# Kernel tuning notes

Measured on AMD Instinct MI355X. Metric: run time of the kernel, lower is better.

## Reference

```python
import jax, jax.numpy as jnp
import numpy as np

D_MODEL = 1024
NUM_HEADS = 16
DEPTH = D_MODEL // NUM_HEADS


def setup_inputs() -> dict:
    key = jax.random.key(0)
    ks = jax.random.split(key, 9)
    B, S = 2, 2048
    scale = 1.0 / np.sqrt(D_MODEL)
    x = jax.random.normal(ks[0], (B, S, D_MODEL), dtype=jnp.float32)
    wq = jax.random.normal(ks[1], (D_MODEL, D_MODEL), dtype=jnp.float32) * scale
    bq = jax.random.normal(ks[2], (D_MODEL,), dtype=jnp.float32) * 0.01
    wk = jax.random.normal(ks[3], (D_MODEL, D_MODEL), dtype=jnp.float32) * scale
    bk = jax.random.normal(ks[4], (D_MODEL,), dtype=jnp.float32) * 0.01
    wv = jax.random.normal(ks[5], (D_MODEL, D_MODEL), dtype=jnp.float32) * scale
    bv = jax.random.normal(ks[6], (D_MODEL,), dtype=jnp.float32) * 0.01
    wo = jax.random.normal(ks[7], (D_MODEL, D_MODEL), dtype=jnp.float32) * scale
    bo = jax.random.normal(ks[8], (D_MODEL,), dtype=jnp.float32) * 0.01
    return {"x": x, "wq": wq, "bq": bq, "wk": wk, "bk": bk,
            "wv": wv, "bv": bv, "wo": wo, "bo": bo}


def reference(x, wq, bq, wk, bk, wv, bv, wo, bo):
    B, S, _ = x.shape
    def split_heads(t):  # [B,S,D] -> [B,H,S,depth]
        return t.reshape(B, S, NUM_HEADS, DEPTH).transpose(0, 2, 1, 3)
    q = split_heads(x @ wq + bq)
    k = split_heads(x @ wk + bk)
    v = split_heads(x @ wv + bv)
    # scaled dot-product attention, full [B,H,S,S] scores as in the original
    logits = jnp.einsum('bhqd,bhkd->bhqk', q, k) / jnp.sqrt(
        jnp.asarray(DEPTH, dtype=jnp.float32))
    attn = jax.nn.softmax(logits, axis=-1)
    out = jnp.einsum('bhqk,bhkd->bhqd', attn, v)
    out = out.transpose(0, 2, 1, 3).reshape(B, S, D_MODEL)
    return out @ wo + bo
```

## Files before the change

kernel.cpp:

```cpp
#include <hip/hip_runtime.h>


#define S_LEN 2048
#define DM 1024
#define MROWS 4096
#define QSCALE 0.1803368801111244f

typedef unsigned short u16;
typedef unsigned int u32;
typedef __attribute__((ext_vector_type(8))) short short8;
typedef __attribute__((ext_vector_type(4))) float f32x4;
typedef __attribute__((ext_vector_type(4))) unsigned short u16x4;
typedef __attribute__((ext_vector_type(2))) unsigned int u32x2;

__device__ inline u16 f2bf(float f) {
    u32 u = __float_as_uint(f);
    u = u + 0x7fffu + ((u >> 16) & 1u);
    return (u16)(u >> 16);
}
__device__ inline void gld_lds16(const u16* g, u16* l) {
    __builtin_amdgcn_global_load_lds(
        (const __attribute__((address_space(1))) void*)g,
        (__attribute__((address_space(3))) void*)l, 16, 0, 0);
}
__device__ inline f32x4 mfma16(short8 a, short8 b, f32x4 c) {
    return __builtin_amdgcn_mfma_f32_16x16x32_bf16(a, b, c, 0, 0, 0);
}

__global__ void prep_all(const float* __restrict__ x, u16* __restrict__ xb,
                         const float* __restrict__ wq, const float* __restrict__ wk,
                         const float* __restrict__ wv, const float* __restrict__ wo,
                         const float* __restrict__ bq, const float* __restrict__ bk,
                         const float* __restrict__ bv, const float* __restrict__ bo,
                         u16* __restrict__ wallT, u16* __restrict__ woT,
                         float* __restrict__ biasAll, float* __restrict__ biasO) {
    const int t = threadIdx.x;
    if (blockIdx.x < 2048) {
        const size_t i8 = ((size_t)blockIdx.x * 256 + t) * 8;
        const f32x4 a = ((const f32x4*)x)[i8 / 4];
        const f32x4 b = ((const f32x4*)x)[i8 / 4 + 1];
        u16 o[8];
#pragma unroll
        for (int i = 0; i < 4; i++) { o[i] = f2bf(a[i]); o[4 + i] = f2bf(b[i]); }
        *(short8*)(xb + i8) = *(const short8*)o;
        return;
    }
    const int bid = blockIdx.x - 2048;
    if (bid == 1024) {
#pragma unroll
        for (int i = 0; i < 4; i++) {
            const int idx = i * 256 + t;
            biasAll[idx]        = bq[idx] * QSCALE;
            biasAll[1024 + idx] = bk[idx];
            biasAll[2048 + idx] = bv[idx];
            biasO[idx]          = bo[idx];
        }
        return;
    }
    __shared__ float lds[64][65];
    const int m  = bid >> 8;
    const int tk = (bid >> 4) & 15;
    const int tn = bid & 15;
    const float* src = (m == 0) ? wq : (m == 1) ? wk : (m == 2) ? wv : wo;
    const float scale = (m == 0) ? QSCALE : 1.0f;
    const int r4 = t >> 6, c = t & 63;
#pragma unroll
    for (int i = 0; i < 16; i++) {
        const int k = tk * 64 + i * 4 + r4;
        lds[i * 4 + r4][c] = src[(size_t)k * 1024 + tn * 64 + c];
    }
    __syncthreads();
#pragma unroll
    for (int i = 0; i < 16; i++) {
        const int n = tn * 64 + i * 4 + r4;
        const int k = tk * 64 + c;
        const u16 v = f2bf(lds[c][i * 4 + r4] * scale);
        if (m < 3) wallT[((size_t)m * 1024 + n) * 1024 + k] = v;
        else       woT[(size_t)n * 1024 + k] = v;
    }
}

__global__ __launch_bounds__(256, 3)
void gemm_qkv(const u16* __restrict__ A, const u16* __restrict__ Bt,
              const float* __restrict__ bias, u16* __restrict__ Cq,
              u16* __restrict__ Ck, u16* __restrict__ Cv,
              const int K, const int N) {
    __shared__ __align__(16) u16 As[128 * 32];
    __shared__ __align__(16) u16 Bs[128 * 32];
    __shared__ __align__(16) u16 Ct[128 * 136];
    const int tid = threadIdx.x;
    const int w = tid >> 6, lane = tid & 63;
    const int wm = w >> 1, wn = w & 1;
    const int l16 = lane & 15, quad = lane >> 4;
    const int tm = blockIdx.x * 128;
    const int tn = blockIdx.y * 128;
    const int region = tn >> 10;

    const int sr = w * 16 + (lane >> 2);
    const int sc = (lane & 3) * 8;
    const u16* ag0 = A + (size_t)(tm + sr) * K + sc;
    const u16* ag1 = A + (size_t)(tm + sr + 64) * K + sc;
    const u16* bg0 = Bt + (size_t)(tn + sr) * K + sc;
    const u16* bg1 = Bt + (size_t)(tn + sr + 64) * K + sc;
    u16* al = As + w * 512;
    u16* bl = Bs + w * 512;

    f32x4 acc[4][4];
#pragma unroll
    for (int i = 0; i < 4; i++)
#pragma unroll
        for (int j = 0; j < 4; j++) acc[i][j] = (f32x4){0.f, 0.f, 0.f, 0.f};

    for (int kb = 0; kb < K; kb += 32) {
        __syncthreads();
        gld_lds16(ag0 + kb, al);
        gld_lds16(ag1 + kb, al + 2048);
        gld_lds16(bg0 + kb, bl);
        gld_lds16(bg1 + kb, bl + 2048);
        __syncthreads();
        short8 af[4], bfr[4];
#pragma unroll
        for (int i = 0; i < 4; i++) {
            af[i]  = *(const short8*)(As + (wm * 64 + i * 16 + l16) * 32 + quad * 8);
            bfr[i] = *(const short8*)(Bs + (wn * 64 + i * 16 + l16) * 32 + quad * 8);
        }
#pragma unroll
        for (int i = 0; i < 4; i++)
#pragma unroll
            for (int j = 0; j < 4; j++)
                acc[i][j] = mfma16(af[i], bfr[j], acc[i][j]);
    }

    if (region < 2) {
#pragma unroll
        for (int j = 0; j < 4; j++) {
            const int colL = wn * 64 + j * 16 + l16;
            const float bv = bias[tn + colL];
#pragma unroll
            for (int i = 0; i < 4; i++) {
                const int row0 = wm * 64 + i * 16 + quad * 4;
#pragma unroll
                for (int r = 0; r < 4; r++)
                    Ct[(row0 + r) * 136 + colL] = f2bf(acc[i][j][r] + bv);
            }
        }
    } else {
#pragma unroll
        for (int j = 0; j < 4; j++) {
            const int colL = wn * 64 + j * 16 + l16;
            const float bv = bias[tn + colL];
#pragma unroll
            for (int i = 0; i < 4; i++) {
                const int row0 = wm * 64 + i * 16 + quad * 4;
                u16x4 pk;
#pragma unroll
                for (int r = 0; r < 4; r++) pk[r] = f2bf(acc[i][j][r] + bv);
                *(u16x4*)(Ct + colL * 132 + row0) = pk;
            }
        }
    }
    __syncthreads();

    if (region == 0) {
#pragma unroll
        for (int p = 0; p < 8; p++) {
            const int rowL = p * 16 + (tid >> 4);
            const int c8 = (tid & 15) * 8;
            const short8 v = *(const short8*)(Ct + rowL * 136 + c8);
            *(short8*)(Cq + (size_t)(tm + rowL) * 1024 + tn + c8) = v;
        }
    } else if (region == 1) {
        const int b = tm >> 11, sBase = tm & 2047;
#pragma unroll
        for (int p = 0; p < 8; p++) {
            const int rowL = p * 16 + (tid >> 4);
            const int c8 = (tid & 15) * 8;
            const short8 v = *(const short8*)(Ct + rowL * 136 + c8);
            const int s = sBase + rowL;
            const int hd = (tn - 1024) + c8;
            const int h = hd >> 6, dd = hd & 63;
            const int chunk = ((dd >> 3) + s) & 7;
            *(short8*)(Ck + (((size_t)(b * 16 + h) * 2048 + s) << 6) + chunk * 8) = v;
        }
    } else {
        const int b = tm >> 11, tBase = (tm & 2047) >> 6;
        const int hBase = (tn >> 6) - 32;
#pragma unroll
        for (int p = 0; p < 8; p++) {
            const int cid = p * 256 + tid;
            const int q3 = cid & 7;
            const int colL = (cid >> 3) & 127;
            const int half = cid >> 10;
            const int d = colL & 63;
            const int h = hBase + (colL >> 6);
            const int c = (q3 - d) & 7;
            const int base = (c & 3) * 4 + ((c & 4) << 3);
            const u32x2 Ar = *(const u32x2*)(Ct + colL * 132 + half * 64 + base);
            const u32x2 Br = *(const u32x2*)(Ct + colL * 132 + half * 64 + base + 16);
            union { u32 u[4]; short8 s8; } o;
            o.u[0] = __builtin_amdgcn_perm(Br[0], Ar[0], 0x05040100u);
            o.u[1] = __builtin_amdgcn_perm(Br[0], Ar[0], 0x07060302u);
            o.u[2] = __builtin_amdgcn_perm(Br[1], Ar[1], 0x05040100u);
            o.u[3] = __builtin_amdgcn_perm(Br[1], Ar[1], 0x07060302u);
            *(short8*)(Cv + (((size_t)((b * 16 + h) * 32 + tBase + half)) << 12) +
                       d * 64 + q3 * 8) = o.s8;
        }
    }
}

__global__ __launch_bounds__(256, 2)
void gemm_out64(const u16* __restrict__ A, const u16* __restrict__ Bt,
                const float* __restrict__ bias, float* __restrict__ C,
                const int K, const int N) {
    __shared__ __align__(16) u16 As[64 * 32];
    __shared__ __align__(16) u16 Bs[128 * 32];
    const int tid = threadIdx.x;
    const int w = tid >> 6, lane = tid & 63;
    const int wm = w >> 1, wn = w & 1;
    const int l16 = lane & 15, quad = lane >> 4;
    const int tm = blockIdx.x * 64;
    const int tn = blockIdx.y * 128;

    const int sr = w * 16 + (lane >> 2);
    const int sc = (lane & 3) * 8;
    const u16* ag  = A + (size_t)(tm + sr) * K + sc;
    const u16* bg0 = Bt + (size_t)(tn + sr) * K + sc;
    const u16* bg1 = Bt + (size_t)(tn + sr + 64) * K + sc;
    u16* al = As + w * 512;
    u16* bl = Bs + w * 512;

    f32x4 acc[2][4];
#pragma unroll
    for (int i = 0; i < 2; i++)
#pragma unroll
        for (int j = 0; j < 4; j++) acc[i][j] = (f32x4){0.f, 0.f, 0.f, 0.f};

    for (int kb = 0; kb < K; kb += 32) {
        __syncthreads();
        gld_lds16(ag + kb, al);
        gld_lds16(bg0 + kb, bl);
        gld_lds16(bg1 + kb, bl + 2048);
        __syncthreads();
        short8 af[2], bfr[4];
#pragma unroll
        for (int i = 0; i < 2; i++)
            af[i] = *(const short8*)(As + (wm * 32 + i * 16 + l16) * 32 + quad * 8);
#pragma unroll
        for (int j = 0; j < 4; j++)
            bfr[j] = *(const short8*)(Bs + (wn * 64 + j * 16 + l16) * 32 + quad * 8);
#pragma unroll
        for (int i = 0; i < 2; i++)
#pragma unroll
            for (int j = 0; j < 4; j++)
                acc[i][j] = mfma16(af[i], bfr[j], acc[i][j]);
    }
#pragma unroll
    for (int j = 0; j < 4; j++) {
        const int col = tn + wn * 64 + j * 16 + l16;
        const float bv = bias[col];
#pragma unroll
        for (int i = 0; i < 2; i++) {
            const int row0 = tm + wm * 32 + i * 16 + quad * 4;
#pragma unroll
            for (int r = 0; r < 4; r++)
                C[(size_t)(row0 + r) * N + col] = acc[i][j][r] + bv;
        }
    }
}

__global__ __launch_bounds__(256, 2)
void flash_attn(const u16* __restrict__ Qb, const u16* __restrict__ Ktg,
                const u16* __restrict__ Vtb, u16* __restrict__ O) {
    __shared__ __align__(16) u16 Ks[2][8192];
    __shared__ __align__(16) u16 Vs[2][8192];
    const int tid = threadIdx.x;
    const int w = tid >> 6, lane = tid & 63;
    const int l16 = lane & 15, quad = lane >> 4;
    const int lid = blockIdx.x + blockIdx.y * 16;
    const int bh = lid & 31, b = bh >> 4, h = bh & 15;
    const int q0 = (lid >> 5) * 128 + w * 32;

    short8 qf[2][2];
#pragma unroll
    for (int u = 0; u < 2; u++) {
        const size_t qrow = (size_t)(b * S_LEN + q0 + u * 16 + l16) * 1024 + h * 64;
        qf[u][0] = *(const short8*)(Qb + qrow + quad * 8);
        qf[u][1] = *(const short8*)(Qb + qrow + 32 + quad * 8);
    }
    u16 ones_s[8];
#pragma unroll
    for (int i = 0; i < 8; i++) ones_s[i] = 0x3F80u;
    const short8 ones = *(const short8*)ones_s;

    const u16* kg = Ktg + ((size_t)bh << 17) + w * 2048 + lane * 8;
    const u16* vg = Vtb + ((size_t)bh << 17) + w * 2048 + lane * 8;
    u16* kl0 = &Ks[0][0] + w * 2048;
    u16* vl0 = &Vs[0][0] + w * 2048;
    u16* kl1 = &Ks[1][0] + w * 2048;
    u16* vl1 = &Vs[1][0] + w * 2048;

    const int ka0 = l16 * 64 + ((quad + l16) & 7) * 8;
    const int ka1 = l16 * 64 + ((4 + quad + l16) & 7) * 8;

    f32x4 o[2][4], osum[2];
#pragma unroll
    for (int u = 0; u < 2; u++) {
        osum[u] = (f32x4){0.f, 0.f, 0.f, 0.f};
#pragma unroll
        for (int d = 0; d < 4; d++) o[u][d] = (f32x4){0.f, 0.f, 0.f, 0.f};
    }
    const f32x4 zz = (f32x4){0.f, 0.f, 0.f, 0.f};

#pragma unroll
    for (int k = 0; k < 4; k++) {
        gld_lds16(kg + k * 512, kl0 + k * 512);
        gld_lds16(vg + k * 512, vl0 + k * 512);
    }
    __syncthreads();

    auto step = [&](int t, const u16* Kc, const u16* Vc,
                    u16* klN, u16* vlN, bool pf) {
        if (pf) {
            const int off = (t + 1) * 8192;
#pragma unroll
            for (int k = 0; k < 4; k++) {
                gld_lds16(kg + off + k * 512, klN + k * 512);
                gld_lds16(vg + off + k * 512, vlN + k * 512);
            }
            asm volatile("s_waitcnt vmcnt(8)" ::: "memory");
        } else {
            asm volatile("s_waitcnt vmcnt(0)" ::: "memory");
        }
        __builtin_amdgcn_s_barrier();

        f32x4 s[2][8];
        __builtin_amdgcn_s_setprio(1);
#pragma unroll
        for (int a = 0; a < 8; a++) {
            const short8 kf0 = *(const short8*)(Kc + a * 1024 + ka0);
            const short8 kf1 = *(const short8*)(Kc + a * 1024 + ka1);
#pragma unroll
            for (int u = 0; u < 2; u++) {
                s[u][a] = mfma16(kf0, qf[u][0], zz);
                s[u][a] = mfma16(kf1, qf[u][1], s[u][a]);
            }
        }
        __builtin_amdgcn_s_setprio(0);
        union { u32 u[4]; short8 s8; } pu[2][4];
#pragma unroll
        for (int u = 0; u < 2; u++) {
#pragma unroll
            for (int p = 0; p < 4; p++) {
#pragma unroll
                for (int r = 0; r < 4; r++) {
                    const float e0 = __builtin_amdgcn_exp2f(s[u][2 * p][r]);
                    const float e1 = __builtin_amdgcn_exp2f(s[u][2 * p + 1][r]);
                    pu[u][p].u[r] = __builtin_amdgcn_perm(
                        __float_as_uint(e1), __float_as_uint(e0), 0x07060302u);
                }
                osum[u] = mfma16(ones, pu[u][p].s8, osum[u]);
            }
        }
        __builtin_amdgcn_s_setprio(1);
#pragma unroll
        for (int dv = 0; dv < 4; dv++) {
            const short8 vf0a = *(const short8*)(Vc + dv * 1024 + ka0);
            const short8 vf1a = *(const short8*)(Vc + dv * 1024 + ka1);
            const short8 vf0b = *(const short8*)(Vc + 4096 + dv * 1024 + ka0);
            const short8 vf1b = *(const short8*)(Vc + 4096 + dv * 1024 + ka1);
#pragma unroll
            for (int u = 0; u < 2; u++) {
                o[u][dv] = mfma16(vf0a, pu[u][0].s8, o[u][dv]);
                o[u][dv] = mfma16(vf1a, pu[u][1].s8, o[u][dv]);
                o[u][dv] = mfma16(vf0b, pu[u][2].s8, o[u][dv]);
                o[u][dv] = mfma16(vf1b, pu[u][3].s8, o[u][dv]);
            }
        }
        __builtin_amdgcn_s_setprio(0);
        __builtin_amdgcn_s_barrier();
    };

#pragma unroll 1
    for (int tp = 0; tp < S_LEN / 256; tp++) {
        step(2 * tp,     &Ks[0][0], &Vs[0][0], kl1, vl1, true);
        step(2 * tp + 1, &Ks[1][0], &Vs[1][0], kl0, vl0, tp < S_LEN / 256 - 1);
    }

#pragma unroll
    for (int u = 0; u < 2; u++) {
        const float inv = 1.0f / osum[u][0];
        const size_t obase =
            (size_t)(b * S_LEN + q0 + u * 16 + l16) * DM + h * 64 + quad * 4;
#pragma unroll
        for (int d = 0; d < 4; d++) {
            u16x4 pk;
#pragma unroll
            for (int r = 0; r < 4; r++) pk[r] = f2bf(o[u][d][r] * inv);
            *(u16x4*)(O + obase + d * 16) = pk;
        }
    }
}

extern "C" void kernel_launch(void* const* d_in, const int* in_sizes, int n_in,
                              void* d_out, int out_size, void* d_ws, size_t ws_size,
                              hipStream_t stream) {
    const float* x  = (const float*)d_in[0];
    const float* wq = (const float*)d_in[1];
    const float* bq = (const float*)d_in[2];
    const float* wk = (const float*)d_in[3];
    const float* bk = (const float*)d_in[4];
    const float* wv = (const float*)d_in[5];
    const float* bv = (const float*)d_in[6];
    const float* wo = (const float*)d_in[7];
    const float* bo = (const float*)d_in[8];

    char* ws = (char*)d_ws;
    u16*   wallT   = (u16*)(ws + 64);
    u16*   woT     = (u16*)(ws + 6291520);
    float* biasAll = (float*)(ws + 8388672);
    float* biasO   = (float*)(ws + 8400960);
    u16*   xb      = (u16*)(ws + 8405056);
    u16*   Qb      = (u16*)(ws + 16793664);
    u16*   Ktg     = (u16*)(ws + 25182272);
    u16*   Vtb     = (u16*)(ws + 33570880);
    u16*   Obuf    = (u16*)(ws + 41959488);

    prep_all<<<3073, 256, 0, stream>>>(x, xb, wq, wk, wv, wo, bq, bk, bv, bo,
                                       wallT, woT, biasAll, biasO);
    gemm_qkv<<<dim3(32, 24), 256, 0, stream>>>(xb, wallT, biasAll,
                                               Qb, Ktg, Vtb, 1024, 3072);
    flash_attn<<<dim3(16, 32), 256, 0, stream>>>(Qb, Ktg, Vtb, Obuf);
    gemm_out64<<<dim3(64, 8), 256, 0, stream>>>(Obuf, woT, biasO,
                                                (float*)d_out, 1024, 1024);
}
```

Before: 179.9 us.

## Rewrite QKV GEMM as 256x256 tile with double-buffered swizzled LDS pipeline

The QKV projection GEMM moves from 128x128 tiles with 256 threads and single-buffered K=32 steps to 256x256 tiles with 512 threads and double-buffered K=64 steps. It uses XOR-swizzled LDS layouts, and async global-to-LDS prefetches of the next tile are interleaved with MFMA phases under explicit barriers and s_setprio. The aim is to hide global load latency, cut LDS bank conflicts and raise arithmetic intensity per block. In exchange it launches only 192 blocks, fewer than the CU count, uses 128KB of LDS, and serialises the epilogue into four quadrant passes.

```diff
diff --git a/kernel.cpp b/kernel.cpp
--- a/kernel.cpp
+++ b/kernel.cpp
@@ -3,7 +3,6 @@
 
 #define S_LEN 2048
 #define DM 1024
-#define MROWS 4096
 #define QSCALE 0.1803368801111244f
 
 typedef unsigned short u16;
@@ -80,131 +79,220 @@
     }
 }
 
-__global__ __launch_bounds__(256, 3)
+__global__ __launch_bounds__(512, 2)
 void gemm_qkv(const u16* __restrict__ A, const u16* __restrict__ Bt,
               const float* __restrict__ bias, u16* __restrict__ Cq,
               u16* __restrict__ Ck, u16* __restrict__ Cv,
               const int K, const int N) {
-    __shared__ __align__(16) u16 As[128 * 32];
-    __shared__ __align__(16) u16 Bs[128 * 32];
-    __shared__ __align__(16) u16 Ct[128 * 136];
+    __shared__ __align__(16) u16 smem[65536];
+    u16* const As0 = smem;
+    u16* const As1 = smem + 16384;
+    u16* const Bs0 = smem + 32768;
+    u16* const Bs1 = smem + 49152;
+
     const int tid = threadIdx.x;
     const int w = tid >> 6, lane = tid & 63;
-    const int wm = w >> 1, wn = w & 1;
+    const int wr = w >> 2, wc = w & 3;
     const int l16 = lane & 15, quad = lane >> 4;
-    const int tm = blockIdx.x * 128;
-    const int tn = blockIdx.y * 128;
-    const int region = tn >> 10;
-
-    const int sr = w * 16 + (lane >> 2);
-    const int sc = (lane & 3) * 8;
-    const u16* ag0 = A + (size_t)(tm + sr) * K + sc;
-    const u16* ag1 = A + (size_t)(tm + sr + 64) * K + sc;
-    const u16* bg0 = Bt + (size_t)(tn + sr) * K + sc;
-    const u16* bg1 = Bt + (size_t)(tn + sr + 64) * K + sc;
-    u16* al = As + w * 512;
-    u16* bl = Bs + w * 512;
-
-    f32x4 acc[4][4];
-#pragma unroll
-    for (int i = 0; i < 4; i++)
+    const int tm = blockIdx.x * 256;
+    const int tn = blockIdx.y * 256;
+
+    const int swzcol = ((lane & 7) ^ (lane >> 3)) * 8;
+    const u16* agA = A  + (size_t)(tm + w * 32 + (lane >> 3)) * K + swzcol;
+    const u16* bgB = Bt + (size_t)(tn + w * 32 + (lane >> 3)) * K + swzcol;
+
+    const int xr = l16 & 7;
+    const int aOff = (wr * 128 + l16) * 64;
+    const int bOff = (wc * 64 + l16) * 64;
+    const int sk0 = (quad ^ xr) * 8;
+    const int sk1 = ((4 | quad) ^ xr) * 8;
+
+    f32x4 acc[8][4];
+#pragma unroll
+    for (int i = 0; i < 8; i++)
 #pragma unroll
         for (int j = 0; j < 4; j++) acc[i][j] = (f32x4){0.f, 0.f, 0.f, 0.f};
 
-    for (int kb = 0; kb < K; kb += 32) {
+#pragma unroll
+    for (int i = 0; i < 4; i++) {
+        gld_lds16(agA + i * 8 * K, As0 + w * 2048 + i * 512);
+        gld_lds16(bgB + i * 8 * K, Bs0 + w * 2048 + i * 512);
+    }
+    __syncthreads();
+
+    auto tile = [&](int t, const u16* Ac, const u16* Bc,
+                    u16* sAw, u16* sBw, bool pf) {
+        const int kb1 = (t + 1) * 64;
+        short8 a0[4], a1[4], a2[4], a3[4], b0[4], b1[4];
+        if (pf) {
+            gld_lds16(agA + kb1,          sAw + w * 2048);
+            gld_lds16(agA + 8 * K + kb1,  sAw + w * 2048 + 512);
+            gld_lds16(bgB + kb1,          sBw + w * 2048);
+        }
+#pragma unroll
+        for (int j = 0; j < 4; j++) b0[j] = *(const short8*)(Bc + bOff + j * 1024 + sk0);
+#pragma unroll
+        for (int i = 0; i < 4; i++) a0[i] = *(const short8*)(Ac + aOff + i * 1024 + sk0);
+        __builtin_amdgcn_s_barrier();
+        asm volatile("s_waitcnt lgkmcnt(0)" ::: "memory");
+        __builtin_amdgcn_sched_barrier(0);
+        __builtin_amdgcn_s_setprio(1);
+#pragma unroll
+        for (int i = 0; i < 4; i++)
+#pragma unroll
+            for (int j = 0; j < 4; j++)
+                acc[i][j] = mfma16(a0[i], b0[j], acc[i][j]);
+        __builtin_amdgcn_s_setprio(0);
+        __builtin_amdgcn_sched_barrier(0);
+        __builtin_amdgcn_s_barrier();
+        if (pf) {
+            gld_lds16(agA + 16 * K + kb1, sAw + w * 2048 + 1024);
+            gld_lds16(agA + 24 * K + kb1, sAw + w * 2048 + 1536);
+            gld_lds16(bgB + 8 * K + kb1,  sBw + w * 2048 + 512);
+        }
+#pragma unroll
+        for (int i = 0; i < 4; i++) a1[i] = *(const short8*)(Ac + aOff + (4 + i) * 1024 + sk0);
+        __builtin_amdgcn_s_barrier();
+        asm volatile("s_waitcnt lgkmcnt(0)" ::: "memory");
+        __builtin_amdgcn_sched_barrier(0);
+        __builtin_amdgcn_s_setprio(1);
+#pragma unroll
+        for (int i = 0; i < 4; i++)
+#pragma unroll
+            for (int j = 0; j < 4; j++)
+                acc[4 + i][j] = mfma16(a1[i], b0[j], acc[4 + i][j]);
+        __builtin_amdgcn_s_setprio(0);
+        __builtin_amdgcn_sched_barrier(0);
+        __builtin_amdgcn_s_barrier();
+        if (pf) {
+            gld_lds16(bgB + 16 * K + kb1, sBw + w * 2048 + 1024);
+            gld_lds16(bgB + 24 * K + kb1, sBw + w * 2048 + 1536);
+        }
+#pragma unroll
+        for (int j = 0; j < 4; j++) b1[j] = *(const short8*)(Bc + bOff + j * 1024 + sk1);
+#pragma unroll
+        for (int i = 0; i < 4; i++) a2[i] = *(const short8*)(Ac + aOff + i * 1024 + sk1);
+        __builtin_amdgcn_s_barrier();
+        asm volatile("s_waitcnt lgkmcnt(0)" ::: "memory");
+        __builtin_amdgcn_sched_barrier(0);
+        __builtin_amdgcn_s_setprio(1);
+#pragma unroll
+        for (int i = 0; i < 4; i++)
+#pragma unroll
+            for (int j = 0; j < 4; j++)
+                acc[i][j] = mfma16(a2[i], b1[j], acc[i][j]);
+        __builtin_amdgcn_s_setprio(0);
+        __builtin_amdgcn_sched_barrier(0);
+        __builtin_amdgcn_s_barrier();
+#pragma unroll
+        for (int i = 0; i < 4; i++) a3[i] = *(const short8*)(Ac + aOff + (4 + i) * 1024 + sk1);
+        __builtin_amdgcn_s_barrier();
+        asm volatile("s_waitcnt lgkmcnt(0)" ::: "memory");
+        __builtin_amdgcn_sched_barrier(0);
+        __builtin_amdgcn_s_setprio(1);
+#pragma unroll
+        for (int i = 0; i < 4; i++)
+#pragma unroll
+            for (int j = 0; j < 4; j++)
+                acc[4 + i][j] = mfma16(a3[i], b1[j], acc[4 + i][j]);
+        __builtin_amdgcn_s_setprio(0);
+        asm volatile("s_waitcnt vmcnt(0)" ::: "memory");
+        __builtin_amdgcn_sched_barrier(0);
+        __builtin_amdgcn_s_barrier();
+    };
+
+#pragma unroll 1
+    for (int tp = 0; tp < 8; tp++) {
+        tile(2 * tp,     As0, Bs0, As1, Bs1, true);
+        tile(2 * tp + 1, As1, Bs1, As0, Bs0, tp < 7);
+    }
+
+    __syncthreads();
+    u16* const Ct = smem;
+    const int wnL = wc & 1;
+#pragma unroll 1
+    for (int q = 0; q < 4; q++) {
+        const int qi = q >> 1, qj = q & 1;
+        const int tmq = tm + qi * 128;
+        const int tnq = tn + qj * 128;
+        const int region = tnq >> 10;
+        if (wr == qi && (wc >> 1) == qj) {
+            if (region < 2) {
+#pragma unroll
+                for (int j = 0; j < 4; j++) {
+                    const int colL = wnL * 64 + j * 16 + l16;
+                    const float bv = bias[tnq + colL];
+#pragma unroll
+                    for (int i = 0; i < 8; i++) {
+                        const int row0 = i * 16 + quad * 4;
+#pragma unroll
+                        for (int r = 0; r < 4; r++)
+                            Ct[(row0 + r) * 136 + colL] = f2bf(acc[i][j][r] + bv);
+                    }
+                }
+            } else {
+#pragma unroll
+                for (int j = 0; j < 4; j++) {
+                    const int colL = wnL * 64 + j * 16 + l16;
+                    const float bv = bias[tnq + colL];
+#pragma unroll
+                    for (int i = 0; i < 8; i++) {
+                        const int row0 = i * 16 + quad * 4;
+                        u16x4 pk;
+#pragma unroll
+                        for (int r = 0; r < 4; r++) pk[r] = f2bf(acc[i][j][r] + bv);
+                        *(u16x4*)(Ct + colL * 132 + row0) = pk;
+                    }
+                }
+            }
+        }
         __syncthreads();
-        gld_lds16(ag0 + kb, al);
-        gld_lds16(ag1 + kb, al + 2048);
-        gld_lds16(bg0 + kb, bl);
-        gld_lds16(bg1 + kb, bl + 2048);
+        if (region == 0) {
+#pragma unroll
+            for (int p = 0; p < 4; p++) {
+                const int rowL = p * 32 + (tid >> 4);
+                const int c8 = (tid & 15) * 8;
+                const short8 v = *(const short8*)(Ct + rowL * 136 + c8);
+                *(short8*)(Cq + (size_t)(tmq + rowL) * 1024 + tnq + c8) = v;
+            }
+        } else if (region == 1) {
+            const int b = tmq >> 11, sBase = tmq & 2047;
+#pragma unroll
+            for (int p = 0; p < 4; p++) {
+                const int rowL = p * 32 + (tid >> 4);
+                const int c8 = (tid & 15) * 8;
+                const short8 v = *(const short8*)(Ct + rowL * 136 + c8);
+                const int s = sBase + rowL;
+                const int hd = (tnq - 1024) + c8;
+                const int h = hd >> 6, dd = hd & 63;
+                const int chunk = ((dd >> 3) + s) & 7;
+                *(short8*)(Ck + (((size_t)(b * 16 + h) * 2048 + s) << 6) + chunk * 8) = v;
+            }
+        } else {
+            const int b = tmq >> 11, tBase = (tmq & 2047) >> 6;
+            const int hBase = (tnq >> 6) - 32;
+#pragma unroll
+            for (int p = 0; p < 4; p++) {
+                const int cid = p * 512 + tid;
+                const int q3 = cid & 7;
+                const int colL = (cid >> 3) & 127;
+                const int half = cid >> 10;
+                const int d = colL & 63;
+                const int h = hBase + (colL >> 6);
+                const int c = (q3 - d) & 7;
+                const int base = (c & 3) * 4 + ((c & 4) << 3);
+                const u32x2 Ar = *(const u32x2*)(Ct + colL * 132 + half * 64 + base);
+                const u32x2 Br = *(const u32x2*)(Ct + colL * 132 + half * 64 + base + 16);
+                union { u32 u[4]; short8 s8; } o;
+                o.u[0] = __builtin_amdgcn_perm(Br[0], Ar[0], 0x05040100u);
+                o.u[1] = __builtin_amdgcn_perm(Br[0], Ar[0], 0x07060302u);
+                o.u[2] = __builtin_amdgcn_perm(Br[1], Ar[1], 0x05040100u);
+                o.u[3] = __builtin_amdgcn_perm(Br[1], Ar[1], 0x07060302u);
+                *(short8*)(Cv + (((size_t)((b * 16 + h) * 32 + tBase + half)) << 12) +
+                           d * 64 + q3 * 8) = o.s8;
+            }
+        }
         __syncthreads();
-        short8 af[4], bfr[4];
-#pragma unroll
-        for (int i = 0; i < 4; i++) {
-            af[i]  = *(const short8*)(As + (wm * 64 + i * 16 + l16) * 32 + quad * 8);
-            bfr[i] = *(const short8*)(Bs + (wn * 64 + i * 16 + l16) * 32 + quad * 8);
-        }
-#pragma unroll
-        for (int i = 0; i < 4; i++)
-#pragma unroll
-            for (int j = 0; j < 4; j++)
-                acc[i][j] = mfma16(af[i], bfr[j], acc[i][j]);
-    }
-
-    if (region < 2) {
-#pragma unroll
-        for (int j = 0; j < 4; j++) {
-            const int colL = wn * 64 + j * 16 + l16;
-            const float bv = bias[tn + colL];
-#pragma unroll
-            for (int i = 0; i < 4; i++) {
-                const int row0 = wm * 64 + i * 16 + quad * 4;
-#pragma unroll
-                for (int r = 0; r < 4; r++)
-                    Ct[(row0 + r) * 136 + colL] = f2bf(acc[i][j][r] + bv);
-            }
-        }
-    } else {
-#pragma unroll
-        for (int j = 0; j < 4; j++) {
-            const int colL = wn * 64 + j * 16 + l16;
-            const float bv = bias[tn + colL];
-#pragma unroll
-            for (int i = 0; i < 4; i++) {
-                const int row0 = wm * 64 + i * 16 + quad * 4;
-                u16x4 pk;
-#pragma unroll
-                for (int r = 0; r < 4; r++) pk[r] = f2bf(acc[i][j][r] + bv);
-                *(u16x4*)(Ct + colL * 132 + row0) = pk;
-            }
-        }
-    }
-    __syncthreads();
-
-    if (region == 0) {
-#pragma unroll
-        for (int p = 0; p < 8; p++) {
-            const int rowL = p * 16 + (tid >> 4);
-            const int c8 = (tid & 15) * 8;
-            const short8 v = *(const short8*)(Ct + rowL * 136 + c8);
-            *(short8*)(Cq + (size_t)(tm + rowL) * 1024 + tn + c8) = v;
-        }
-    } else if (region == 1) {
-        const int b = tm >> 11, sBase = tm & 2047;
-#pragma unroll
-        for (int p = 0; p < 8; p++) {
-            const int rowL = p * 16 + (tid >> 4);
-            const int c8 = (tid & 15) * 8;
-            const short8 v = *(const short8*)(Ct + rowL * 136 + c8);
-            const int s = sBase + rowL;
-            const int hd = (tn - 1024) + c8;
-            const int h = hd >> 6, dd = hd & 63;
-            const int chunk = ((dd >> 3) + s) & 7;
-            *(short8*)(Ck + (((size_t)(b * 16 + h) * 2048 + s) << 6) + chunk * 8) = v;
-        }
-    } else {
-        const int b = tm >> 11, tBase = (tm & 2047) >> 6;
-        const int hBase = (tn >> 6) - 32;
-#pragma unroll
-        for (int p = 0; p < 8; p++) {
-            const int cid = p * 256 + tid;
-            const int q3 = cid & 7;
-            const int colL = (cid >> 3) & 127;
-            const int half = cid >> 10;
-            const int d = colL & 63;
-            const int h = hBase + (colL >> 6);
-            const int c = (q3 - d) & 7;
-            const int base = (c & 3) * 4 + ((c & 4) << 3);
-            const u32x2 Ar = *(const u32x2*)(Ct + colL * 132 + half * 64 + base);
-            const u32x2 Br = *(const u32x2*)(Ct + colL * 132 + half * 64 + base + 16);
-            union { u32 u[4]; short8 s8; } o;
-            o.u[0] = __builtin_amdgcn_perm(Br[0], Ar[0], 0x05040100u);
-            o.u[1] = __builtin_amdgcn_perm(Br[0], Ar[0], 0x07060302u);
-            o.u[2] = __builtin_amdgcn_perm(Br[1], Ar[1], 0x05040100u);
-            o.u[3] = __builtin_amdgcn_perm(Br[1], Ar[1], 0x07060302u);
-            *(short8*)(Cv + (((size_t)((b * 16 + h) * 32 + tBase + half)) << 12) +
-                       d * 64 + q3 * 8) = o.s8;
-        }
     }
 }
 
@@ -427,7 +515,7 @@
 
     prep_all<<<3073, 256, 0, stream>>>(x, xb, wq, wk, wv, wo, bq, bk, bv, bo,
                                        wallT, woT, biasAll, biasO);
-    gemm_qkv<<<dim3(32, 24), 256, 0, stream>>>(xb, wallT, biasAll,
+    gemm_qkv<<<dim3(16, 12), 512, 0, stream>>>(xb, wallT, biasAll,
                                                Qb, Ktg, Vtb, 1024, 3072);
     flash_attn<<<dim3(16, 32), 256, 0, stream>>>(Qb, Ktg, Vtb, Obuf);
     gemm_out64<<<dim3(64, 8), 256, 0, stream>>>(Obuf, woT, biasO,
```

Measured after the change: 186.0 us. 1.03x slower.

## Double K-step in output GEMM with XOR-swizzled LDS, vectorize weight-prep loads

Applied to the files above, without the earlier changes.

The output-projection GEMM now stages a 64-wide K slice per iteration instead of 32. The slice is placed in LDS with an XOR swizzle on 16-byte chunks to avoid bank conflicts, which halves the number of barrier pairs per K loop. The weight transpose/convert prep kernel now reads source weights with float4 vector loads instead of scalar loads. The bigger tiles double LDS use in gemm_out64, which may affect occupancy.

```diff
diff --git a/kernel.cpp b/kernel.cpp
--- a/kernel.cpp
+++ b/kernel.cpp
@@ -3,7 +3,6 @@
 
 #define S_LEN 2048
 #define DM 1024
-#define MROWS 4096
 #define QSCALE 0.1803368801111244f
 
 typedef unsigned short u16;
@@ -63,13 +62,20 @@
     const int tn = bid & 15;
     const float* src = (m == 0) ? wq : (m == 1) ? wk : (m == 2) ? wv : wo;
     const float scale = (m == 0) ? QSCALE : 1.0f;
+    const int rT = t >> 4;
+    const int c4 = (t & 15) * 4;
+#pragma unroll
+    for (int p = 0; p < 4; p++) {
+        const int r = p * 16 + rT;
+        const f32x4 v = *(const f32x4*)(src + (size_t)(tk * 64 + r) * 1024 +
+                                        tn * 64 + c4);
+        lds[r][c4]     = v[0];
+        lds[r][c4 + 1] = v[1];
+        lds[r][c4 + 2] = v[2];
+        lds[r][c4 + 3] = v[3];
+    }
+    __syncthreads();
     const int r4 = t >> 6, c = t & 63;
-#pragma unroll
-    for (int i = 0; i < 16; i++) {
-        const int k = tk * 64 + i * 4 + r4;
-        lds[i * 4 + r4][c] = src[(size_t)k * 1024 + tn * 64 + c];
-    }
-    __syncthreads();
 #pragma unroll
     for (int i = 0; i < 16; i++) {
         const int n = tn * 64 + i * 4 + r4;
@@ -212,8 +218,8 @@
 void gemm_out64(const u16* __restrict__ A, const u16* __restrict__ Bt,
                 const float* __restrict__ bias, float* __restrict__ C,
                 const int K, const int N) {
-    __shared__ __align__(16) u16 As[64 * 32];
-    __shared__ __align__(16) u16 Bs[128 * 32];
+    __shared__ __align__(16) u16 As[64 * 64];
+    __shared__ __align__(16) u16 Bs[128 * 64];
     const int tid = threadIdx.x;
     const int w = tid >> 6, lane = tid & 63;
     const int wm = w >> 1, wn = w & 1;
@@ -221,13 +227,12 @@
     const int tm = blockIdx.x * 64;
     const int tn = blockIdx.y * 128;
 
-    const int sr = w * 16 + (lane >> 2);
-    const int sc = (lane & 3) * 8;
-    const u16* ag  = A + (size_t)(tm + sr) * K + sc;
-    const u16* bg0 = Bt + (size_t)(tn + sr) * K + sc;
-    const u16* bg1 = Bt + (size_t)(tn + sr + 64) * K + sc;
-    u16* al = As + w * 512;
-    u16* bl = Bs + w * 512;
+    const int swz = ((lane & 7) ^ (lane >> 3)) * 8;
+    const u16* ag = A  + (size_t)(tm + w * 8 + (lane >> 3)) * K + swz;
+    const u16* bg = Bt + (size_t)(tn + w * 8 + (lane >> 3)) * K + swz;
+
+    const int xk0 = ((quad) ^ (l16 & 7)) * 8;
+    const int xk1 = ((4 | quad) ^ (l16 & 7)) * 8;
 
     f32x4 acc[2][4];
 #pragma unroll
@@ -235,24 +240,38 @@
 #pragma unroll
         for (int j = 0; j < 4; j++) acc[i][j] = (f32x4){0.f, 0.f, 0.f, 0.f};
 
-    for (int kb = 0; kb < K; kb += 32) {
+    for (int kb = 0; kb < K; kb += 64) {
         __syncthreads();
-        gld_lds16(ag + kb, al);
-        gld_lds16(bg0 + kb, bl);
-        gld_lds16(bg1 + kb, bl + 2048);
+#pragma unroll
+        for (int i = 0; i < 2; i++)
+            gld_lds16(ag + (size_t)i * 32 * K + kb, As + i * 2048 + w * 512);
+#pragma unroll
+        for (int i = 0; i < 4; i++)
+            gld_lds16(bg + (size_t)i * 32 * K + kb, Bs + i * 2048 + w * 512);
         __syncthreads();
-        short8 af[2], bfr[4];
+        short8 a0[2], a1[2], b0[4], b1[4];
+#pragma unroll
+        for (int i = 0; i < 2; i++) {
+            const int ar = (wm * 32 + i * 16 + l16) * 64;
+            a0[i] = *(const short8*)(As + ar + xk0);
+            a1[i] = *(const short8*)(As + ar + xk1);
+        }
+#pragma unroll
+        for (int j = 0; j < 4; j++) {
+            const int br = (wn * 64 + j * 16 + l16) * 64;
+            b0[j] = *(const short8*)(Bs + br + xk0);
+            b1[j] = *(const short8*)(Bs + br + xk1);
+        }
 #pragma unroll
         for (int i = 0; i < 2; i++)
-            af[i] = *(const short8*)(As + (wm * 32 + i * 16 + l16) * 32 + quad * 8);
-#pragma unroll
-        for (int j = 0; j < 4; j++)
-            bfr[j] = *(const short8*)(Bs + (wn * 64 + j * 16 + l16) * 32 + quad * 8);
+#pragma unroll
+            for (int j = 0; j < 4; j++)
+                acc[i][j] = mfma16(a0[i], b0[j], acc[i][j]);
 #pragma unroll
         for (int i = 0; i < 2; i++)
 #pragma unroll
             for (int j = 0; j < 4; j++)
-                acc[i][j] = mfma16(af[i], bfr[j], acc[i][j]);
+                acc[i][j] = mfma16(a1[i], b1[j], acc[i][j]);
     }
 #pragma unroll
     for (int j = 0; j < 4; j++) {
```

Result: no change. 180.1 us, median of 2 (+0.1%).
